# Performance work log

Hardware: AMD Instinct MI355X
Metric: run time of the kernel (lower is better)

Reference implementation:

```python
import jax, jax.numpy as jnp
import numpy as np

TOP_K = 2

def setup_inputs() -> dict:
    key = jax.random.key(0)
    k1, k2, k3, k4 = jax.random.split(key, 4)
    B, S, D, E = 4, 4096, 2048, 8
    x = jax.random.normal(k1, (B, S, D), dtype=jnp.float32)
    w_g = jax.random.normal(k2, (E, D), dtype=jnp.float32) * (1.0 / np.sqrt(D))
    w_noise = jax.random.normal(k3, (E, D), dtype=jnp.float32) * (1.0 / np.sqrt(D))
    eps = jax.random.normal(k4, (B, S, E), dtype=jnp.float32)
    return {"x": x, "w_g": w_g, "w_noise": w_noise, "eps": eps}

def reference(x, w_g, w_noise, eps):
    # gate logits: [B, S, E]
    logits = jnp.einsum('bsd,ed->bse', x, w_g)
    # noisy top-k: logits += softplus(x @ w_noise.T) * eps
    noise = jax.nn.softplus(jnp.einsum('bsd,ed->bse', x, w_noise)) * eps
    logits = logits + noise
    top_k_logits, top_k_indices = jax.lax.top_k(logits, TOP_K)
    return (top_k_logits, top_k_indices)
```

## Files before the change

### kernel.cpp

```cpp
#include <hip/hip_runtime.h>
#include <math.h>

#define TOKENS 16384
#define DIM 2048
#define NE 8
#define BLOCK 512
#define GRID 256
#define NCHUNK (DIM / 256)
#define NGRP 2

__launch_bounds__(BLOCK, 2)
__global__ void router_kernel(const float* __restrict__ x,
                              const float* __restrict__ w_g,
                              const float* __restrict__ w_noise,
                              const float* __restrict__ eps,
                              float* __restrict__ out)
{
    __shared__ float wlds[16 * DIM];
    __shared__ float nbuf[NGRP][4][64];

    const int tid = threadIdx.x;

    {
        const float4* g4 = (const float4*)w_g;
        const float4* n4 = (const float4*)w_noise;
        float4* l4 = (float4*)wlds;
        #pragma unroll
        for (int i = tid; i < (NE * DIM) / 4; i += BLOCK) {
            l4[i] = g4[i];
            l4[i + (NE * DIM) / 4] = n4[i];
        }
    }
    __syncthreads();

    const int lane  = tid & 63;
    const int wv    = tid >> 6;
    const int pair  = wv >> 1;
    const int noisy = wv & 1;

    const float4* x4  = (const float4*)x;
    const float4* wl4 = (const float4*)wlds + (noisy ? (NE * DIM / 4) : 0);

    const int e = lane >> 3;
    const int t = lane & 7;

    for (int g = 0; g < NGRP; ++g) {
        const int tok0 = blockIdx.x * 64 + g * 32 + pair * 8;

        float ev = 0.f;
        if (noisy) ev = eps[(tok0 + t) * NE + e];

        float V[64];
        #pragma unroll
        for (int v = 0; v < 64; ++v) V[v] = 0.f;

        float4 xv[8];
        #pragma unroll
        for (int tt = 0; tt < 8; ++tt)
            xv[tt] = x4[(tok0 + tt) * (DIM / 4) + lane];

        #pragma unroll
        for (int k = 0; k < NCHUNK; ++k) {
            float4 xn[8];
            if (k < NCHUNK - 1) {
                #pragma unroll
                for (int tt = 0; tt < 8; ++tt)
                    xn[tt] = x4[(tok0 + tt) * (DIM / 4) + (k + 1) * 64 + lane];
            }
            #pragma unroll
            for (int r = 0; r < 8; ++r) {
                const float4 w = wl4[r * (DIM / 4) + k * 64 + lane];
                #pragma unroll
                for (int tt = 0; tt < 8; ++tt) {
                    float a = V[r * 8 + tt];
                    a = fmaf(xv[tt].x, w.x, a);
                    a = fmaf(xv[tt].y, w.y, a);
                    a = fmaf(xv[tt].z, w.z, a);
                    a = fmaf(xv[tt].w, w.w, a);
                    V[r * 8 + tt] = a;
                }
            }
            if (k < NCHUNK - 1) {
                #pragma unroll
                for (int tt = 0; tt < 8; ++tt) xv[tt] = xn[tt];
            }
        }

        #pragma unroll
        for (int s = 0; s < 6; ++s) {
            const int m = 1 << s;
            const int n = 64 >> s;
            #pragma unroll
            for (int j = 0; j < n / 2; ++j) {
                const float A = V[2 * j];
                const float B = V[2 * j + 1];
                const float As = __shfl_xor(A, m, 64);
                const float Bs = __shfl_xor(B, m, 64);
                V[j] = (lane & m) ? (B + Bs) : (A + As);
            }
        }
        const float mine = V[0];

        if (noisy) {
            const float sp = fmaxf(mine, 0.f) + log1pf(expf(-fabsf(mine)));
            nbuf[g][pair][lane] = sp * ev;
        }
        __syncthreads();
        if (!noisy) {
            const float logit = mine + nbuf[g][pair][lane];

            float v1 = logit, v2 = -INFINITY;
            int   i1 = e,     i2 = 7;
            #pragma unroll
            for (int sm = 3; sm <= 5; ++sm) {
                const int m = 1 << sm;
                const float ov1 = __shfl_xor(v1, m, 64);
                const float ov2 = __shfl_xor(v2, m, 64);
                const int   oi1 = __shfl_xor(i1, m, 64);
                const int   oi2 = __shfl_xor(i2, m, 64);
                const bool firstA = (v1 > ov1) || (v1 == ov1 && i1 < oi1);
                const float nv1 = firstA ? v1  : ov1;
                const int   ni1 = firstA ? i1  : oi1;
                const float ca  = firstA ? ov1 : v1;
                const int   cia = firstA ? oi1 : i1;
                const float cb  = firstA ? v2  : ov2;
                const int   cib = firstA ? i2  : oi2;
                const bool secondA = (ca > cb) || (ca == cb && cia < cib);
                v1 = nv1; i1 = ni1;
                v2 = secondA ? ca : cb;
                i2 = secondA ? cia : cib;
            }

            if (e == 0) {
                const int tok = tok0 + t;
                *(float2*)&out[2 * tok] = make_float2(v1, v2);
                *(float2*)&out[2 * TOKENS + 2 * tok] = make_float2((float)i1, (float)i2);
            }
        }
    }
}

extern "C" void kernel_launch(void* const* d_in, const int* in_sizes, int n_in,
                              void* d_out, int out_size, void* d_ws, size_t ws_size,
                              hipStream_t stream) {
    const float* x       = (const float*)d_in[0];
    const float* w_g     = (const float*)d_in[1];
    const float* w_noise = (const float*)d_in[2];
    const float* eps     = (const float*)d_in[3];
    float* out = (float*)d_out;

    router_kernel<<<GRID, BLOCK, 0, stream>>>(x, w_g, w_noise, eps, out);
}
```

Measured before the change: 36.70 us.

## Split expert rows across more waves to cut registers and raise occupancy

Doubles the block to 1024 threads so each wave computes 4 expert rows instead of 8. This halves the per-thread accumulator array and drops the software x prefetch to lower register pressure. Both gate and noise results now go through a shared buffer and one wave per quad does the top-k. Each x tile is now loaded by four waves instead of two, and the per-group synchronisation is block-wide across more waves.

```diff
diff --git a/kernel.cpp b/kernel.cpp
--- a/kernel.cpp
+++ b/kernel.cpp
@@ -4,12 +4,12 @@
 #define TOKENS 16384
 #define DIM 2048
 #define NE 8
-#define BLOCK 512
+#define BLOCK 1024
 #define GRID 256
 #define NCHUNK (DIM / 256)
 #define NGRP 2
 
-__launch_bounds__(BLOCK, 2)
+__launch_bounds__(BLOCK, 4)
 __global__ void router_kernel(const float* __restrict__ x,
                               const float* __restrict__ w_g,
                               const float* __restrict__ w_noise,
@@ -17,7 +17,7 @@
                               float* __restrict__ out)
 {
     __shared__ float wlds[16 * DIM];
-    __shared__ float nbuf[NGRP][4][64];
+    __shared__ float lbuf[NGRP][4][2][NE][8];
 
     const int tid = threadIdx.x;
 
@@ -25,7 +25,6 @@
         const float4* g4 = (const float4*)w_g;
         const float4* n4 = (const float4*)w_noise;
         float4* l4 = (float4*)wlds;
-        #pragma unroll
         for (int i = tid; i < (NE * DIM) / 4; i += BLOCK) {
             l4[i] = g4[i];
             l4[i + (NE * DIM) / 4] = n4[i];
@@ -33,42 +32,37 @@
     }
     __syncthreads();
 
-    const int lane  = tid & 63;
-    const int wv    = tid >> 6;
-    const int pair  = wv >> 1;
-    const int noisy = wv & 1;
+    const int lane    = tid & 63;
+    const int wv      = tid >> 6;
+    const int quad    = wv >> 2;
+    const int noisy   = (wv >> 1) & 1;
+    const int rowhalf = wv & 1;
 
     const float4* x4  = (const float4*)x;
-    const float4* wl4 = (const float4*)wlds + (noisy ? (NE * DIM / 4) : 0);
+    const float4* wl4 = (const float4*)wlds + (noisy * NE + rowhalf * 4) * (DIM / 4);
 
-    const int e = lane >> 3;
-    const int t = lane & 7;
+    const int eloc = (lane >> 3) & 3;
+    const int e    = rowhalf * 4 + eloc;
+    const int t    = lane & 7;
 
     for (int g = 0; g < NGRP; ++g) {
-        const int tok0 = blockIdx.x * 64 + g * 32 + pair * 8;
+        const int tok0 = blockIdx.x * 64 + g * 32 + quad * 8;
 
         float ev = 0.f;
-        if (noisy) ev = eps[(tok0 + t) * NE + e];
+        if (noisy && lane < 32) ev = eps[(tok0 + t) * NE + e];
 
-        float V[64];
+        float V[32];
         #pragma unroll
-        for (int v = 0; v < 64; ++v) V[v] = 0.f;
+        for (int v = 0; v < 32; ++v) V[v] = 0.f;
 
-        float4 xv[8];
-        #pragma unroll
-        for (int tt = 0; tt < 8; ++tt)
-            xv[tt] = x4[(tok0 + tt) * (DIM / 4) + lane];
-
-        #pragma unroll
+        #pragma unroll 2
         for (int k = 0; k < NCHUNK; ++k) {
-            float4 xn[8];
-            if (k < NCHUNK - 1) {
-                #pragma unroll
-                for (int tt = 0; tt < 8; ++tt)
-                    xn[tt] = x4[(tok0 + tt) * (DIM / 4) + (k + 1) * 64 + lane];
-            }
+            float4 xv[8];
             #pragma unroll
-            for (int r = 0; r < 8; ++r) {
+            for (int tt = 0; tt < 8; ++tt)
+                xv[tt] = x4[(tok0 + tt) * (DIM / 4) + k * 64 + lane];
+            #pragma unroll
+            for (int r = 0; r < 4; ++r) {
                 const float4 w = wl4[r * (DIM / 4) + k * 64 + lane];
                 #pragma unroll
                 for (int tt = 0; tt < 8; ++tt) {
@@ -80,16 +74,12 @@
                     V[r * 8 + tt] = a;
                 }
             }
-            if (k < NCHUNK - 1) {
-                #pragma unroll
-                for (int tt = 0; tt < 8; ++tt) xv[tt] = xn[tt];
-            }
         }
 
         #pragma unroll
-        for (int s = 0; s < 6; ++s) {
+        for (int s = 0; s < 5; ++s) {
             const int m = 1 << s;
-            const int n = 64 >> s;
+            const int n = 32 >> s;
             #pragma unroll
             for (int j = 0; j < n / 2; ++j) {
                 const float A = V[2 * j];
@@ -99,18 +89,24 @@
                 V[j] = (lane & m) ? (B + Bs) : (A + As);
             }
         }
-        const float mine = V[0];
+        const float mine = V[0] + __shfl_xor(V[0], 32, 64);
 
-        if (noisy) {
-            const float sp = fmaxf(mine, 0.f) + log1pf(expf(-fabsf(mine)));
-            nbuf[g][pair][lane] = sp * ev;
+        if (lane < 32) {
+            if (noisy) {
+                const float sp = fmaxf(mine, 0.f) + log1pf(expf(-fabsf(mine)));
+                lbuf[g][quad][1][e][t] = sp * ev;
+            } else {
+                lbuf[g][quad][0][e][t] = mine;
+            }
         }
         __syncthreads();
-        if (!noisy) {
-            const float logit = mine + nbuf[g][pair][lane];
+
+        if ((wv & 3) == 0) {
+            const int te = lane >> 3;
+            const float logit = lbuf[g][quad][0][te][t] + lbuf[g][quad][1][te][t];
 
             float v1 = logit, v2 = -INFINITY;
-            int   i1 = e,     i2 = 7;
+            int   i1 = te,    i2 = 7;
             #pragma unroll
             for (int sm = 3; sm <= 5; ++sm) {
                 const int m = 1 << sm;
@@ -131,7 +127,7 @@
                 i2 = secondA ? cia : cib;
             }
 
-            if (e == 0) {
+            if (te == 0) {
                 const int tok = tok0 + t;
                 *(float2*)&out[2 * tok] = make_float2(v1, v2);
                 *(float2*)&out[2 * TOKENS + 2 * tok] = make_float2((float)i1, (float)i2);
```

After: 34.86 us. -5.0%, faster.
